# Kernel tuning notes

Measured on AMD Instinct MI355X. Metric: run time of the kernel, lower is better.

## Reference

```python
import jax, jax.numpy as jnp
import numpy as np

B, T, E, H = 256, 256, 64, 4  # batch, num_trees, embedding_size, hidden_size


def setup_inputs() -> dict:
    key = jax.random.key(0)
    k1, k2, k3 = jax.random.split(key, 3)
    x = jax.random.normal(k1, (B, 1, T, E), dtype=jnp.float32)
    W1 = jax.random.normal(k2, (T, T, E, H), dtype=jnp.float32) * 0.01  # linear1 (leading 1 dropped)
    b1 = jnp.zeros((T, T, H), dtype=jnp.float32)
    W2 = jax.random.normal(k3, (T, (T - 1) * H, E), dtype=jnp.float32) * 0.01  # linear2
    b2 = jnp.zeros((T, E), dtype=jnp.float32)
    return {"x": x, "W1": W1, "b1": b1, "W2": W2, "b2": b2}


def _offdiag_idx(num_trees):
    # For each output tree i, the column indices j != i (static, shape [T, T-1]).
    mask = ~np.eye(num_trees, dtype=bool)
    return jnp.asarray(np.nonzero(mask)[1].reshape(num_trees, num_trees - 1))


def reference(x, W1, b1, W2, b2):
    num_trees, hidden = W1.shape[0], W1.shape[-1]
    x0 = x[:, 0]  # (B, T, E): broadcast dim removed; x[b,0,j,e] pairs with W1[i,j,e,h]
    # Locally-connected layer 1: per-pair (i,j) contraction over embedding dim e.
    h = jax.nn.relu(jnp.einsum('bje,ijeh->bijh', x0, W1) + b1)  # (B, T, T, H)
    # Dropout(p=0.5) is identity in eval mode.
    # masked_select(~eye): drop the diagonal j == i via a static gather.
    idx = _offdiag_idx(num_trees)  # (T, T-1)
    h2 = jnp.take_along_axis(h, idx[None, :, :, None], axis=2)  # (B, T, T-1, H)
    h2 = h2.reshape(h.shape[0], num_trees, (num_trees - 1) * hidden)
    # Locally-connected layer 2: per-tree i contraction over the (T-1)*H dim.
    out = jnp.einsum('btk,tke->bte', h2, W2) + b2  # (B, T, E)
    return out
```

## Files before the change

### kernel.cpp

```cpp
#include <hip/hip_runtime.h>


namespace {

constexpr int T_ = 256;
constexpr int E_ = 64;
constexpr int K2_ = 1020;

typedef float  f32x4  __attribute__((ext_vector_type(4)));
typedef short  bf16x8 __attribute__((ext_vector_type(8)));
typedef unsigned short u16x4 __attribute__((ext_vector_type(4)));

__device__ inline unsigned short f2b(float f) {
    union { float f; unsigned u; } v; v.f = f;
    unsigned r = v.u + 0x7fffu + ((v.u >> 16) & 1u);
    return (unsigned short)(r >> 16);
}

__device__ inline bf16x8 pack8(f32x4 a, f32x4 b) {
    bf16x8 r;
    r[0] = (short)f2b(a[0]); r[1] = (short)f2b(a[1]);
    r[2] = (short)f2b(a[2]); r[3] = (short)f2b(a[3]);
    r[4] = (short)f2b(b[0]); r[5] = (short)f2b(b[1]);
    r[6] = (short)f2b(b[2]); r[7] = (short)f2b(b[3]);
    return r;
}

__device__ inline void lds_barrier() {
    asm volatile("s_waitcnt lgkmcnt(0)" ::: "memory");
    __builtin_amdgcn_sched_barrier(0);
    __builtin_amdgcn_s_barrier();
    __builtin_amdgcn_sched_barrier(0);
}

constexpr int JC = 4;
constexpr int CHUNKS = 16;
constexpr int W1_ROW   = 72;
constexpr int W1_PLANE = 32 * W1_ROW + 8;
constexpr int PB_ROW   = 24;
constexpr int PB_PLANE = 64 * PB_ROW + 8;
constexpr int W2_ROW   = 16;
constexpr int W2_PLANE = 64 * W2_ROW + 8;

constexpr int SH_PLANE = 128 * 18 + 2;

}


__global__ __launch_bounds__(256) void xcast_kernel(
    const float* __restrict__ x, unsigned short* __restrict__ xT)
{
    const int g     = blockIdx.x * 256 + threadIdx.x;
    const int part  = g & 3;
    const int rowid = g >> 2;
    const int b = rowid >> 8, j = rowid & 255;
    const float* src = x + (size_t)rowid * E_ + part * 16;
    f32x4 v0 = *(const f32x4*)(src);
    f32x4 v1 = *(const f32x4*)(src + 4);
    f32x4 v2 = *(const f32x4*)(src + 8);
    f32x4 v3 = *(const f32x4*)(src + 12);
    unsigned short* dst = xT + ((size_t)j * 256 + b) * E_ + part * 16;
    *(bf16x8*)(dst)     = pack8(v0, v1);
    *(bf16x8*)(dst + 8) = pack8(v2, v3);
}

__global__ __launch_bounds__(256) void init_out_kernel(
    const float* __restrict__ b2, float* __restrict__ out)
{
    const int idx = blockIdx.x * 256 + threadIdx.x;
    ((f32x4*)out)[idx] = ((const f32x4*)b2)[idx & 4095];
}


__global__ __launch_bounds__(512, 2) void w2z_kernel(
    const float* __restrict__ W2, unsigned short* __restrict__ W2Z)
{
    __shared__ __align__(16) unsigned short sT[64][136];
    const int bid = blockIdx.x;
    const int t = bid >> 3, kb = bid & 7;
    const int tid = threadIdx.x;
    {
        const int kl = tid >> 2;
        const int e0 = (tid & 3) << 4;
        const int k  = kb * 128 + kl;
        const int j  = k >> 2, h = k & 3;
        f32x4 v0 = {0,0,0,0}, v1 = {0,0,0,0}, v2 = {0,0,0,0}, v3 = {0,0,0,0};
        if (j != t) {
            const int ksrc = ((j < t) ? j : j - 1) * 4 + h;
            const float* src = W2 + ((size_t)t * K2_ + ksrc) * E_ + e0;
            v0 = *(const f32x4*)(src);
            v1 = *(const f32x4*)(src + 4);
            v2 = *(const f32x4*)(src + 8);
            v3 = *(const f32x4*)(src + 12);
        }
        #pragma unroll
        for (int m = 0; m < 4; ++m) {
            sT[e0 + m     ][kl] = f2b(v0[m]);
            sT[e0 + 4 + m ][kl] = f2b(v1[m]);
            sT[e0 + 8 + m ][kl] = f2b(v2[m]);
            sT[e0 + 12 + m][kl] = f2b(v3[m]);
        }
    }
    __syncthreads();
    {
        const int e  = tid >> 3;
        const int ko = tid & 7;
        const unsigned short* srow = &sT[e][ko * 16];
        bf16x8 a = *(const bf16x8*)(srow);
        bf16x8 b = *(const bf16x8*)(srow + 8);
        unsigned short* dst = W2Z + ((size_t)t * 64 + e) * 1024 + kb * 128 + ko * 16;
        *(bf16x8*)(dst)     = a;
        *(bf16x8*)(dst + 8) = b;
    }
}

__global__ __launch_bounds__(256, 4) void phaseA3_kernel(
    const unsigned short* __restrict__ xT,
    const float* __restrict__ W1,
    const float* __restrict__ b1,
    unsigned short* __restrict__ H,
    int i_gbase)
{
    __shared__ __align__(16) unsigned short sA[2][4][16][72];
    __shared__ __align__(16) unsigned short sHf[4 * SH_PLANE];

    const int bx = blockIdx.x;
    const int jq = ((bx & 7) << 3) | (bx >> 3);
    const int it = blockIdx.y;
    const int bh = blockIdx.z;
    const int j0 = jq * 4;

    const int tid = threadIdx.x;
    const int w = tid >> 6, lane = tid & 63, r16 = lane & 15, kg = lane >> 4;
    const int bW = w * 32;

    bf16x8 xf[4][2][2];
    #pragma unroll
    for (int j = 0; j < 4; ++j)
        #pragma unroll
        for (int nt = 0; nt < 2; ++nt) {
            const unsigned short* xr =
                xT + ((size_t)(j0 + j) * 256 + bh * 128 + bW + nt * 16 + r16) * 64 + kg * 8;
            xf[j][nt][0] = *(const bf16x8*)(xr);
            xf[j][nt][1] = *(const bf16x8*)(xr + 32);
        }

    auto stage = [&](int iq, int buf) {
        const int p = tid >> 4, seg = tid & 15;
        const int il = p >> 2, j = p & 3;
        const int ig = i_gbase + it * 16 + iq * 4 + il;
        const float* src = W1 + (((size_t)ig * 256 + (j0 + j)) << 8) + seg * 16;
        f32x4 v0 = *(const f32x4*)(src);
        f32x4 v1 = *(const f32x4*)(src + 4);
        f32x4 v2 = *(const f32x4*)(src + 8);
        f32x4 v3 = *(const f32x4*)(src + 12);
        #pragma unroll
        for (int h = 0; h < 4; ++h) {
            u16x4 pk = (u16x4){f2b(v0[h]), f2b(v1[h]), f2b(v2[h]), f2b(v3[h])};
            *(u16x4*)&sA[buf][j][il * 4 + h][seg * 4] = pk;
        }
    };

    auto flushH = [&](int iq) {
        #pragma unroll
        for (int t4 = 0; t4 < 4; ++t4) {
            const int idx = t4 * 256 + tid;
            const int q   = idx & 1;
            const int b   = (idx >> 1) & 127;
            const int il  = idx >> 8;
            const unsigned short* srow = &sHf[il * SH_PLANE + b * 18 + q * 8];
            uint4 v;
            v.x = *(const unsigned*)(srow);
            v.y = *(const unsigned*)(srow + 2);
            v.z = *(const unsigned*)(srow + 4);
            v.w = *(const unsigned*)(srow + 6);
            const int i = it * 16 + iq * 4 + il;
            *(uint4*)(H + (((size_t)i * 64 + jq) * 256 + bh * 128 + b) * 16 + q * 8) = v;
        }
    };

    stage(0, 0);
    lds_barrier();

    for (int iq = 0; iq < 4; ++iq) {
        const int buf = iq & 1;
        if (iq + 1 < 4) stage(iq + 1, buf ^ 1);
        if (iq > 0) flushH(iq - 1);
        lds_barrier();

        #pragma unroll
        for (int j = 0; j < 4; ++j) {
            const unsigned short* ar = &sA[buf][j][r16][0];
            bf16x8 a0 = *(const bf16x8*)(ar + kg * 8);
            bf16x8 a1 = *(const bf16x8*)(ar + 32 + kg * 8);
            const int ig = i_gbase + it * 16 + iq * 4 + kg;
            f32x4 bias = *(const f32x4*)(b1 + (((size_t)ig << 8) + (j0 + j)) * 4);
            #pragma unroll
            for (int nt = 0; nt < 2; ++nt) {
                f32x4 acc = (f32x4){0.f, 0.f, 0.f, 0.f};
                acc = __builtin_amdgcn_mfma_f32_16x16x32_bf16(a0, xf[j][nt][0], acc, 0, 0, 0);
                acc = __builtin_amdgcn_mfma_f32_16x16x32_bf16(a1, xf[j][nt][1], acc, 0, 0, 0);
                float v0 = acc[0] + bias[0]; v0 = v0 > 0.f ? v0 : 0.f;
                float v1 = acc[1] + bias[1]; v1 = v1 > 0.f ? v1 : 0.f;
                float v2 = acc[2] + bias[2]; v2 = v2 > 0.f ? v2 : 0.f;
                float v3 = acc[3] + bias[3]; v3 = v3 > 0.f ? v3 : 0.f;
                unsigned short* dst =
                    &sHf[kg * SH_PLANE + (bW + nt * 16 + r16) * 18 + j * 4];
                *(unsigned*)(dst)     = (unsigned)f2b(v0) | ((unsigned)f2b(v1) << 16);
                *(unsigned*)(dst + 2) = (unsigned)f2b(v2) | ((unsigned)f2b(v3) << 16);
            }
        }
        lds_barrier();
    }
    flushH(3);
}

__global__ __launch_bounds__(512, 4) void phaseB_kernel(
    const unsigned short* __restrict__ H,
    const unsigned short* __restrict__ W2Z,
    const float* __restrict__ b2,
    float* __restrict__ out,
    int i_base)
{
    __shared__ __align__(16) unsigned short sA[2][128][72];
    __shared__ __align__(16) unsigned short sB[2][64][72];

    const int bid = blockIdx.x;
    const int t_loc = bid >> 1;
    const int t  = i_base + t_loc;
    const int b0 = (bid & 1) << 7;
    const int tid = threadIdx.x;
    const int w = tid >> 6, lane = tid & 63, r16 = lane & 15, kg = lane >> 4;

    auto stageA = [&](int c, int pb) {
        #pragma unroll
        for (int half = 0; half < 2; ++half) {
            const int idx = half * 512 + tid;
            const int q   = idx & 1;
            const int b   = (idx >> 1) & 127;
            const int jql = idx >> 8;
            const unsigned short* src =
                H + (((size_t)t_loc * 64 + c * 4 + jql) * 256 + b0 + b) * 16 + q * 8;
            bf16x8 v = *(const bf16x8*)src;
            *(bf16x8*)&sA[pb][b][jql * 16 + q * 8] = v;
        }
    };
    auto stageB = [&](int c, int pb) {
        const int e = tid >> 3;
        const int q = tid & 7;
        bf16x8 v = *(const bf16x8*)(W2Z + ((size_t)t * 64 + e) * 1024 + c * 64 + q * 8);
        *(bf16x8*)&sB[pb][e][q * 8] = v;
    };

    stageA(0, 0); stageB(0, 0);
    __syncthreads();

    f32x4 acc[4];
    #pragma unroll
    for (int nt = 0; nt < 4; ++nt) acc[nt] = (f32x4){0.f, 0.f, 0.f, 0.f};

    for (int c = 0; c < 16; ++c) {
        const int pb = c & 1;
        if (c + 1 < 16) { stageA(c + 1, pb ^ 1); stageB(c + 1, pb ^ 1); }

        const unsigned short* ar = &sA[pb][w * 16 + r16][0];
        bf16x8 a0 = *(const bf16x8*)(ar + kg * 8);
        bf16x8 a1 = *(const bf16x8*)(ar + 32 + kg * 8);
        #pragma unroll
        for (int nt = 0; nt < 4; ++nt) {
            const unsigned short* br = &sB[pb][nt * 16 + r16][0];
            bf16x8 bb0 = *(const bf16x8*)(br + kg * 8);
            bf16x8 bb1 = *(const bf16x8*)(br + 32 + kg * 8);
            acc[nt] = __builtin_amdgcn_mfma_f32_16x16x32_bf16(a0, bb0, acc[nt], 0, 0, 0);
            acc[nt] = __builtin_amdgcn_mfma_f32_16x16x32_bf16(a1, bb1, acc[nt], 0, 0, 0);
        }
        __syncthreads();
    }

    #pragma unroll
    for (int nt = 0; nt < 4; ++nt) {
        const int e = nt * 16 + r16;
        const float bias = b2[(t << 6) + e];
        #pragma unroll
        for (int r = 0; r < 4; ++r) {
            const int b = b0 + w * 16 + kg * 4 + r;
            out[((size_t)b << 14) + (t << 6) + e] = acc[nt][r] + bias;
        }
    }
}


template <bool XBF>
__global__ __launch_bounds__(512, 4) void fused_forest_kernel(
    const void*  __restrict__ xv,
    const float* __restrict__ W1,
    const float* __restrict__ b1,
    const float* __restrict__ W2,
    float* __restrict__ out)
{
    __shared__ __align__(16) unsigned short sW1[4 * W1_PLANE];
    __shared__ __align__(16) unsigned short sPB[8 * PB_PLANE];
    __shared__ __align__(16) unsigned short sW2[2][8 * W2_PLANE];
    __shared__ __align__(16) float sB1[4][32];

    const int bid = blockIdx.x;
    const int xcd = bid & 7;
    const int rr  = bid >> 3;
    const int tgl = rr >> 4;
    const int bg  = (rr >> 2) & 3;
    const int jg  = rr & 3;
    const int tg  = tgl * 8 + xcd;
    const int i0  = tg << 3;
    const int b0  = bg << 6;
    const int j0g = jg << 6;

    const int tid  = threadIdx.x;
    const int w    = tid >> 6;
    const int lane = tid & 63;
    const int r16  = lane & 15;
    const int kg   = lane >> 4;
    const int bt   = w & 3;
    const int mh   = w >> 2;

    f32x4 acc[4][4];
    #pragma unroll
    for (int mt = 0; mt < 4; ++mt)
        #pragma unroll
        for (int nt = 0; nt < 4; ++nt)
            acc[mt][nt] = (f32x4){0.f, 0.f, 0.f, 0.f};

    auto stage = [&](int c, int pb) {
        const int j0 = j0g + c * JC;
        if (tid < 128) {
            const int jj = tid >> 5, ih = tid & 31;
            sB1[jj][ih] = b1[((i0 + (ih >> 2)) * T_ + (j0 + jj)) * 4 + (ih & 3)];
        }
        {
            const float* src = W1 + (((size_t)(i0 + w) * T_ + (j0 + kg)) * E_) * 4 + r16 * 16;
            f32x4 v0 = *(const f32x4*)(src);
            f32x4 v1 = *(const f32x4*)(src + 4);
            f32x4 v2 = *(const f32x4*)(src + 8);
            f32x4 v3 = *(const f32x4*)(src + 12);
            #pragma unroll
            for (int h = 0; h < 4; ++h) {
                u16x4 pk = (u16x4){f2b(v0[h]), f2b(v1[h]), f2b(v2[h]), f2b(v3[h])};
                *(u16x4*)&sW1[kg * W1_PLANE + (w * 4 + h) * W1_ROW + r16 * 4] = pk;
            }
        }
        {
            const int kk   = lane >> 2;
            const int e0   = (lane & 3) * 16;
            const int tabs = i0 + w;
            const int j    = j0 + (kk >> 2);
            unsigned short* dst = &sW2[pb][w * W2_PLANE + kk];
            if (j == tabs) {
                #pragma unroll
                for (int q = 0; q < 16; ++q) dst[(e0 + q) * W2_ROW] = 0;
            } else {
                const int ksrc = ((j < tabs) ? j : j - 1) * 4 + (kk & 3);
                const float* src = W2 + ((size_t)tabs * K2_ + ksrc) * E_ + e0;
                f32x4 v0 = *(const f32x4*)(src);
                f32x4 v1 = *(const f32x4*)(src + 4);
                f32x4 v2 = *(const f32x4*)(src + 8);
                f32x4 v3 = *(const f32x4*)(src + 12);
                #pragma unroll
                for (int q = 0; q < 4; ++q) {
                    dst[(e0 + q)      * W2_ROW] = f2b(v0[q]);
                    dst[(e0 + 4 + q)  * W2_ROW] = f2b(v1[q]);
                    dst[(e0 + 8 + q)  * W2_ROW] = f2b(v2[q]);
                    dst[(e0 + 12 + q) * W2_ROW] = f2b(v3[q]);
                }
            }
        }
    };

    stage(0, 0);
    __syncthreads();

    const int brow = b0 + bt * 16 + r16;

    for (int c = 0; c < CHUNKS; ++c) {
        const int j0 = j0g + c * JC;
        #pragma unroll
        for (int jj = 0; jj < JC; ++jj) {
            bf16x8 xa, xc;
            if (XBF) {
                const unsigned short* xr =
                    (const unsigned short*)xv + ((size_t)(j0 + jj) * 256 + brow) * E_;
                xa = *(const bf16x8*)(xr + kg * 8);
                xc = *(const bf16x8*)(xr + 32 + kg * 8);
            } else {
                const float* xr = (const float*)xv + ((size_t)brow * T_ + (j0 + jj)) * E_ + kg * 8;
                xa = pack8(*(const f32x4*)xr, *(const f32x4*)(xr + 4));
                xc = pack8(*(const f32x4*)(xr + 32), *(const f32x4*)(xr + 36));
            }
            const unsigned short* wr = &sW1[jj * W1_PLANE + (mh * 16 + r16) * W1_ROW];
            bf16x8 wa = *(const bf16x8*)(wr + kg * 8);
            bf16x8 wc = *(const bf16x8*)(wr + 32 + kg * 8);
            f32x4 cf = (f32x4){0.f, 0.f, 0.f, 0.f};
            cf = __builtin_amdgcn_mfma_f32_16x16x32_bf16(wa, xa, cf, 0, 0, 0);
            cf = __builtin_amdgcn_mfma_f32_16x16x32_bf16(wc, xc, cf, 0, 0, 0);
            const int i = mh * 4 + kg;
            f32x4 bias = *(const f32x4*)&sB1[jj][i * 4];
            #pragma unroll
            for (int r = 0; r < 4; ++r) {
                float vv = cf[r] + bias[r];
                cf[r] = vv > 0.f ? vv : 0.f;
            }
            unsigned p0 = (unsigned)f2b(cf[0]) | ((unsigned)f2b(cf[1]) << 16);
            unsigned p1 = (unsigned)f2b(cf[2]) | ((unsigned)f2b(cf[3]) << 16);
            uint2 pk; pk.x = p0; pk.y = p1;
            *(uint2*)&sPB[i * PB_PLANE + (bt * 16 + r16) * PB_ROW + jj * 4] = pk;
        }
        __syncthreads();

        {
            const bf16x8 z = (bf16x8){0,0,0,0,0,0,0,0};
            const bool lo = (kg < 2);
            bf16x8 a2[4], bb[4];
            #pragma unroll
            for (int mt = 0; mt < 4; ++mt)
                a2[mt] = lo ? *(const bf16x8*)&sPB[w * PB_PLANE + (mt * 16 + r16) * PB_ROW + kg * 8] : z;
            #pragma unroll
            for (int nt = 0; nt < 4; ++nt)
                bb[nt] = lo ? *(const bf16x8*)&sW2[c & 1][w * W2_PLANE + (nt * 16 + r16) * W2_ROW + kg * 8] : z;
            #pragma unroll
            for (int mt = 0; mt < 4; ++mt)
                #pragma unroll
                for (int nt = 0; nt < 4; ++nt)
                    acc[mt][nt] = __builtin_amdgcn_mfma_f32_16x16x32_bf16(
                        a2[mt], bb[nt], acc[mt][nt], 0, 0, 0);
        }

        if (c + 1 < CHUNKS) stage(c + 1, (c + 1) & 1);
        __syncthreads();
    }

    const int tabs = i0 + w;
    #pragma unroll
    for (int mt = 0; mt < 4; ++mt) {
        const int b = b0 + mt * 16 + kg * 4;
        #pragma unroll
        for (int nt = 0; nt < 4; ++nt) {
            const int e = nt * 16 + r16;
            #pragma unroll
            for (int r = 0; r < 4; ++r)
                unsafeAtomicAdd(&out[((size_t)(b + r) * T_ + tabs) * E_ + e],
                                acc[mt][nt][r]);
        }
    }
}


extern "C" void kernel_launch(void* const* d_in, const int* in_sizes, int n_in,
                              void* d_out, int out_size, void* d_ws, size_t ws_size,
                              hipStream_t stream) {
    const float* x  = (const float*)d_in[0];
    const float* W1 = (const float*)d_in[1];
    const float* b1 = (const float*)d_in[2];
    const float* W2 = (const float*)d_in[3];
    const float* b2 = (const float*)d_in[4];
    float* out = (float*)d_out;
    (void)in_sizes; (void)n_in; (void)out_size;

    const size_t xT_b   = 8388608ull;
    const size_t w2z_b  = 33554432ull;
    const size_t H_full = 134217728ull;

    int NS = 0;
    if (d_ws) {
        const int cands[4] = {1, 2, 4, 8};
        for (int ci = 0; ci < 4; ++ci) {
            if (ws_size >= xT_b + w2z_b + H_full / cands[ci]) { NS = cands[ci]; break; }
        }
    }

    if (NS) {
        unsigned short* xT  = (unsigned short*)d_ws;
        unsigned short* W2Z = (unsigned short*)((char*)d_ws + xT_b);
        unsigned short* H   = (unsigned short*)((char*)d_ws + xT_b + w2z_b);

        hipLaunchKernelGGL(xcast_kernel, dim3(1024), dim3(256), 0, stream, x, xT);
        hipLaunchKernelGGL(w2z_kernel, dim3(2048), dim3(512), 0, stream, W2, W2Z);

        const int TS = 256 / NS;
        const int n_it = TS / 16;
        for (int s = 0; s < NS; ++s) {
            hipLaunchKernelGGL(phaseA3_kernel, dim3(64, n_it, 2), dim3(256), 0, stream,
                               xT, W1, b1, H, s * TS);
            hipLaunchKernelGGL(phaseB_kernel, dim3(TS * 2), dim3(512), 0, stream,
                               H, W2Z, b2, out, s * TS);
        }
    } else {
        const bool xbf = d_ws && ws_size >= xT_b;
        hipLaunchKernelGGL(init_out_kernel, dim3(4096), dim3(256), 0, stream, b2, out);
        if (xbf) {
            hipLaunchKernelGGL(xcast_kernel, dim3(1024), dim3(256), 0, stream,
                               x, (unsigned short*)d_ws);
            hipLaunchKernelGGL(fused_forest_kernel<true>, dim3(512), dim3(512), 0, stream,
                               (const void*)d_ws, W1, b1, W2, out);
        } else {
            hipLaunchKernelGGL(fused_forest_kernel<false>, dim3(512), dim3(512), 0, stream,
                               (const void*)x, W1, b1, W2, out);
        }
    }
}
```

Baseline: 112.6 us.

## Process 32 output trees per phase-A block and flush H per wave

```diff
diff --git a/kernel.cpp b/kernel.cpp
--- a/kernel.cpp
+++ b/kernel.cpp
@@ -114,7 +114,7 @@
     }
 }
 
-__global__ __launch_bounds__(256, 4) void phaseA3_kernel(
+__global__ __launch_bounds__(256, 4) void phaseA9_kernel(
     const unsigned short* __restrict__ xT,
     const float* __restrict__ W1,
     const float* __restrict__ b1,
@@ -126,9 +126,10 @@
 
     const int bx = blockIdx.x;
     const int jq = ((bx & 7) << 3) | (bx >> 3);
-    const int it = blockIdx.y;
+    const int itg = blockIdx.y;
     const int bh = blockIdx.z;
     const int j0 = jq * 4;
+    const int i_blk = i_gbase + itg * 32;
 
     const int tid = threadIdx.x;
     const int w = tid >> 6, lane = tid & 63, r16 = lane & 15, kg = lane >> 4;
@@ -145,10 +146,10 @@
             xf[j][nt][1] = *(const bf16x8*)(xr + 32);
         }
 
-    auto stage = [&](int iq, int buf) {
+    auto stage = [&](int t, int buf) {
         const int p = tid >> 4, seg = tid & 15;
         const int il = p >> 2, j = p & 3;
-        const int ig = i_gbase + it * 16 + iq * 4 + il;
+        const int ig = i_blk + t * 4 + il;
         const float* src = W1 + (((size_t)ig * 256 + (j0 + j)) << 8) + seg * 16;
         f32x4 v0 = *(const f32x4*)(src);
         f32x4 v1 = *(const f32x4*)(src + 4);
@@ -161,39 +162,35 @@
         }
     };
 
-    auto flushH = [&](int iq) {
-        #pragma unroll
-        for (int t4 = 0; t4 < 4; ++t4) {
-            const int idx = t4 * 256 + tid;
-            const int q   = idx & 1;
-            const int b   = (idx >> 1) & 127;
-            const int il  = idx >> 8;
-            const unsigned short* srow = &sHf[il * SH_PLANE + b * 18 + q * 8];
+    auto flush_own = [&](int t) {
+        const int bl = bW + (lane >> 1);
+        const int q  = lane & 1;
+        #pragma unroll
+        for (int il = 0; il < 4; ++il) {
+            const unsigned short* srow = &sHf[il * SH_PLANE + bl * 18 + q * 8];
             uint4 v;
             v.x = *(const unsigned*)(srow);
             v.y = *(const unsigned*)(srow + 2);
             v.z = *(const unsigned*)(srow + 4);
             v.w = *(const unsigned*)(srow + 6);
-            const int i = it * 16 + iq * 4 + il;
-            *(uint4*)(H + (((size_t)i * 64 + jq) * 256 + bh * 128 + b) * 16 + q * 8) = v;
+            const int i = itg * 32 + t * 4 + il;
+            *(uint4*)(H + (((size_t)i * 64 + jq) * 256 + bh * 128 + bl) * 16 + q * 8) = v;
         }
     };
 
     stage(0, 0);
     lds_barrier();
 
-    for (int iq = 0; iq < 4; ++iq) {
-        const int buf = iq & 1;
-        if (iq + 1 < 4) stage(iq + 1, buf ^ 1);
-        if (iq > 0) flushH(iq - 1);
-        lds_barrier();
+    for (int t = 0; t < 8; ++t) {
+        const int buf = t & 1;
+        if (t + 1 < 8) stage(t + 1, buf ^ 1);
 
         #pragma unroll
         for (int j = 0; j < 4; ++j) {
             const unsigned short* ar = &sA[buf][j][r16][0];
             bf16x8 a0 = *(const bf16x8*)(ar + kg * 8);
             bf16x8 a1 = *(const bf16x8*)(ar + 32 + kg * 8);
-            const int ig = i_gbase + it * 16 + iq * 4 + kg;
+            const int ig = i_blk + t * 4 + kg;
             f32x4 bias = *(const f32x4*)(b1 + (((size_t)ig << 8) + (j0 + j)) * 4);
             #pragma unroll
             for (int nt = 0; nt < 2; ++nt) {
@@ -210,9 +207,10 @@
                 *(unsigned*)(dst + 2) = (unsigned)f2b(v2) | ((unsigned)f2b(v3) << 16);
             }
         }
+
+        flush_own(t);
         lds_barrier();
     }
-    flushH(3);
 }
 
 __global__ __launch_bounds__(512, 4) void phaseB_kernel(
@@ -484,9 +482,9 @@
         hipLaunchKernelGGL(w2z_kernel, dim3(2048), dim3(512), 0, stream, W2, W2Z);
 
         const int TS = 256 / NS;
-        const int n_it = TS / 16;
+        const int n_itg = TS / 32;
         for (int s = 0; s < NS; ++s) {
-            hipLaunchKernelGGL(phaseA3_kernel, dim3(64, n_it, 2), dim3(256), 0, stream,
+            hipLaunchKernelGGL(phaseA9_kernel, dim3(64, n_itg, 2), dim3(256), 0, stream,
                                xT, W1, b1, H, s * TS);
             hipLaunchKernelGGL(phaseB_kernel, dim3(TS * 2), dim3(512), 0, stream,
                                H, W2Z, b2, out, s * TS);
```

Result: slower. 116.9 us (+3.8%).
